# Optimization experiments

Measured on AMD Instinct MI355X. Metric: run time of the kernel, lower is better.

## Reference

```python
import jax, jax.numpy as jnp
import numpy as np

GROUP_SIZE = 64

def setup_inputs() -> dict:
    key = jax.random.key(0)
    ks = jax.random.split(key, 7)
    T, N, K, NG = 4096, 4096, 11264, 4096 // GROUP_SIZE
    x = jax.random.normal(ks[0], (T, N), dtype=jnp.float32)
    Q = jax.random.randint(ks[1], (K, N), 0, 8, dtype=jnp.int32)  # uint8 3-bit codes
    scales = jax.random.uniform(ks[2], (K, NG), dtype=jnp.float32)
    zeros = jax.random.uniform(ks[3], (K, NG), dtype=jnp.float32) * 7.0
    mu1 = jax.random.uniform(ks[4], (N,), dtype=jnp.float32) + 0.5
    mu2 = jax.random.uniform(ks[5], (K,), dtype=jnp.float32) + 0.5
    bias = jax.random.normal(ks[6], (K,), dtype=jnp.float32)
    return {"x": x, "Q": Q, "scales": scales, "zeros": zeros, "mu1": mu1, "mu2": mu2, "bias": bias}

def reference(x, Q, scales, zeros, mu1, mu2, bias):
    K, N = Q.shape
    ng = scales.shape[1]
    # group-wise dequant: (Q - zero) * scale, groups along N
    Qg = Q.astype(jnp.float32).reshape(K, ng, GROUP_SIZE)
    W_deq_norm = ((Qg - zeros[:, :, None]) * scales[:, :, None]).reshape(K, N)
    # Sinkhorn mu rescale: per-row mu2, per-column mu1
    W_deq = W_deq_norm * mu2[:, None] * mu1[None, :]
    out = x @ W_deq.T + bias
    return out
```

## Files before the change

kernel.cpp:

```cpp
#include <hip/hip_runtime.h>
#include <stdint.h>
#include <stddef.h>


typedef __attribute__((ext_vector_type(8))) short bfrag;
typedef __attribute__((ext_vector_type(4))) float f32x4;
typedef __attribute__((ext_vector_type(4))) int   i32x4;

__device__ __forceinline__ short f2bf(float f) {
    uint32_t u = __float_as_uint(f);
    u += 0x7fffu + ((u >> 16) & 1u);
    return (short)(u >> 16);
}

__device__ __forceinline__ void gload_lds16(const void* g, void* l) {
    __builtin_amdgcn_global_load_lds(
        (const __attribute__((address_space(1))) void*)g,
        (__attribute__((address_space(3))) void*)l,
        16, 0, 0);
}

__global__ void cvt_x_kernel(const float* __restrict__ x,
                             const float* __restrict__ mu1,
                             short* __restrict__ xb, int per ) {
    int i = blockIdx.x * 256 + threadIdx.x;
    int cb = (i % per) * 8;
    const f32x4* xv = (const f32x4*)x;
    f32x4 a = xv[2 * i];
    f32x4 b = xv[2 * i + 1];
    const f32x4* uv = (const f32x4*)(mu1 + cb);
    f32x4 u0 = uv[0];
    f32x4 u1 = uv[1];
    bfrag o;
    o[0] = f2bf(a[0] * u0[0]); o[1] = f2bf(a[1] * u0[1]);
    o[2] = f2bf(a[2] * u0[2]); o[3] = f2bf(a[3] * u0[3]);
    o[4] = f2bf(b[0] * u1[0]); o[5] = f2bf(b[1] * u1[1]);
    o[6] = f2bf(b[2] * u1[2]); o[7] = f2bf(b[3] * u1[3]);
    ((bfrag*)xb)[i] = o;
}

__global__ void deq_w_kernel(const int* __restrict__ Q,
                             const float* __restrict__ scales,
                             const float* __restrict__ zeros,
                             const float* __restrict__ mu2,
                             short* __restrict__ wb,
                             int k0, int N, int NG) {
    int kl = blockIdx.x;
    int kg = k0 + kl;
    int n0 = threadIdx.x << 4;
    int g  = n0 >> 6;
    float s = scales[(size_t)kg * NG + g] * mu2[kg];
    float z = zeros[(size_t)kg * NG + g];
    const i32x4* qv = (const i32x4*)(Q + (size_t)kg * N + n0);
    bfrag* wv = (bfrag*)(wb + (size_t)kl * N + n0);
#pragma unroll
    for (int h = 0; h < 2; h++) {
        i32x4 q0 = qv[2 * h];
        i32x4 q1 = qv[2 * h + 1];
        bfrag o;
        o[0] = f2bf(((float)q0[0] - z) * s);
        o[1] = f2bf(((float)q0[1] - z) * s);
        o[2] = f2bf(((float)q0[2] - z) * s);
        o[3] = f2bf(((float)q0[3] - z) * s);
        o[4] = f2bf(((float)q1[0] - z) * s);
        o[5] = f2bf(((float)q1[1] - z) * s);
        o[6] = f2bf(((float)q1[2] - z) * s);
        o[7] = f2bf(((float)q1[3] - z) * s);
        wv[h] = o;
    }
}

#define BM 128
#define BN 128
#define BK 32

__global__ void gemm_bt_kernel(const short* __restrict__ A,
                               const short* __restrict__ B,
                               const float* __restrict__ bias,
                               float* __restrict__ C,
                               int Kc, int Nout, int col0) {
    __shared__ __attribute__((aligned(16))) short As[BM * BK];
    __shared__ __attribute__((aligned(16))) short Bs[BN * BK];

    const int tid  = threadIdx.x;
    const int lane = tid & 63;
    const int wave = tid >> 6;
    const int wm   = (wave >> 1) * 64;
    const int wn   = (wave & 1) * 64;
    const int bm   = blockIdx.y * BM;
    const int bnl  = blockIdx.x * BN;

    f32x4 acc[4][4];
#pragma unroll
    for (int i = 0; i < 4; i++)
#pragma unroll
        for (int j = 0; j < 4; j++)
            acc[i][j] = (f32x4){0.f, 0.f, 0.f, 0.f};

    const int skc = ((tid & 3) ^ ((tid >> 3) & 3)) * 8;
    const short* gA  = A + (size_t)(bm + (tid >> 2)) * Kc + skc;
    const short* gA2 = gA + (size_t)64 * Kc;
    const short* gB  = B + (size_t)(bnl + (tid >> 2)) * Kc + skc;
    const short* gB2 = gB + (size_t)64 * Kc;
    short* lA  = As + tid * 8;
    short* lA2 = As + 2048 + tid * 8;
    short* lB  = Bs + tid * 8;
    short* lB2 = Bs + 2048 + tid * 8;

    const int r  = lane & 15;
    const int kc = lane >> 4;
    const int sw = (kc ^ ((r >> 1) & 3)) * 8;
    const short* pa = As + (wm + r) * BK + sw;
    const short* pb = Bs + (wn + r) * BK + sw;

    for (int k0 = 0; k0 < Kc; k0 += BK) {
        gload_lds16(gA + k0, lA);
        gload_lds16(gA2 + k0, lA2);
        gload_lds16(gB + k0, lB);
        gload_lds16(gB2 + k0, lB2);
        __syncthreads();

        bfrag af[4], bfv[4];
#pragma unroll
        for (int i = 0; i < 4; i++) af[i]  = *(const bfrag*)(pa + i * 16 * BK);
#pragma unroll
        for (int j = 0; j < 4; j++) bfv[j] = *(const bfrag*)(pb + j * 16 * BK);

#pragma unroll
        for (int i = 0; i < 4; i++)
#pragma unroll
            for (int j = 0; j < 4; j++)
                acc[i][j] = __builtin_amdgcn_mfma_f32_16x16x32_bf16(
                    af[i], bfv[j], acc[i][j], 0, 0, 0);

        __syncthreads();
    }

    const int row0  = bm + wm + (lane >> 4) * 4;
    const int colg0 = col0 + bnl + wn;
#pragma unroll
    for (int j = 0; j < 4; j++) {
        int col  = colg0 + j * 16 + r;
        float bv = bias[col];
#pragma unroll
        for (int i = 0; i < 4; i++) {
            int row = row0 + i * 16;
#pragma unroll
            for (int q = 0; q < 4; q++)
                C[(size_t)(row + q) * Nout + col] = acc[i][j][q] + bv;
        }
    }
}

__global__ void naive_kernel(const float* __restrict__ x, const int* __restrict__ Q,
                             const float* __restrict__ scales, const float* __restrict__ zeros,
                             const float* __restrict__ mu1, const float* __restrict__ mu2,
                             const float* __restrict__ bias, float* __restrict__ out,
                             int T, int N, int K, int NG) {
    long long total = (long long)T * K;
    for (long long idx = blockIdx.x * 256ll + threadIdx.x; idx < total;
         idx += (long long)gridDim.x * 256ll) {
        int t = (int)(idx / K);
        int k = (int)(idx - (long long)t * K);
        float s = 0.f;
        for (int n = 0; n < N; n++) {
            int g = n >> 6;
            float w = ((float)Q[(size_t)k * N + n] - zeros[(size_t)k * NG + g]) *
                      scales[(size_t)k * NG + g];
            s += x[(size_t)t * N + n] * w * mu1[n];
        }
        out[idx] = s * mu2[k] + bias[k];
    }
}

extern "C" void kernel_launch(void* const* d_in, const int* in_sizes, int n_in,
                              void* d_out, int out_size, void* d_ws, size_t ws_size,
                              hipStream_t stream) {
    const float* x      = (const float*)d_in[0];
    const int*   Q      = (const int*)d_in[1];
    const float* scales = (const float*)d_in[2];
    const float* zeros  = (const float*)d_in[3];
    const float* mu1    = (const float*)d_in[4];
    const float* mu2    = (const float*)d_in[5];
    const float* bias   = (const float*)d_in[6];
    float* out = (float*)d_out;

    const int N  = in_sizes[4];
    const int K  = in_sizes[5];
    const int T  = in_sizes[0] / N;
    const int NG = in_sizes[2] / K;

    const size_t xb_bytes  = (size_t)T * N * 2;
    const size_t row_bytes = (size_t)N * 2;

    if (ws_size < xb_bytes + 128 * row_bytes) {
        naive_kernel<<<4096, 256, 0, stream>>>(x, Q, scales, zeros, mu1, mu2,
                                               bias, out, T, N, K, NG);
        return;
    }

    short* xb = (short*)d_ws;
    short* wb = (short*)((char*)d_ws + xb_bytes);
    size_t max_rows = (ws_size - xb_bytes) / row_bytes;
    int CH = (int)((max_rows / 128) * 128);
    if (CH > K) CH = K;

    cvt_x_kernel<<<(T * N / 8) / 256, 256, 0, stream>>>(x, mu1, xb, N / 8);

    for (int c0 = 0; c0 < K; c0 += CH) {
        int rows = (K - c0 < CH) ? (K - c0) : CH;
        deq_w_kernel<<<rows, N / 16, 0, stream>>>(Q, scales, zeros, mu2, wb,
                                                  c0, N, NG);
        dim3 ggrid(rows / BN, T / BM);
        gemm_bt_kernel<<<ggrid, 256, 0, stream>>>(xb, wb, bias, out, N, K, c0);
    }
}
```

Baseline: 804.2 us.

## Fuse weight dequantization into GEMM B-tile loading with register prefetch

Removes the separate dequant kernel and its bf16 weight buffer. The GEMM now loads int32 codes plus per-group scale and zero directly and dequantizes into LDS inside the K loop. The next tile's codes are prefetched into registers to overlap global latency with compute, and a cheaper round-half-up bf16 conversion is used. In exchange, every M-block re-reads int32 codes, which are twice the size of bf16, and redoes the dequant ALU work. That adds global/L2 traffic and VALU pressure in the main loop.

```diff
diff --git a/kernel.cpp b/kernel.cpp
--- a/kernel.cpp
+++ b/kernel.cpp
@@ -11,6 +11,11 @@
     uint32_t u = __float_as_uint(f);
     u += 0x7fffu + ((u >> 16) & 1u);
     return (short)(u >> 16);
+}
+
+__device__ __forceinline__ short f2bfr(float f) {
+    uint32_t u = __float_as_uint(f);
+    return (short)((u + 0x8000u) >> 16);
 }
 
 __device__ __forceinline__ void gload_lds16(const void* g, void* l) {
@@ -39,46 +44,18 @@
     ((bfrag*)xb)[i] = o;
 }
 
-__global__ void deq_w_kernel(const int* __restrict__ Q,
-                             const float* __restrict__ scales,
-                             const float* __restrict__ zeros,
-                             const float* __restrict__ mu2,
-                             short* __restrict__ wb,
-                             int k0, int N, int NG) {
-    int kl = blockIdx.x;
-    int kg = k0 + kl;
-    int n0 = threadIdx.x << 4;
-    int g  = n0 >> 6;
-    float s = scales[(size_t)kg * NG + g] * mu2[kg];
-    float z = zeros[(size_t)kg * NG + g];
-    const i32x4* qv = (const i32x4*)(Q + (size_t)kg * N + n0);
-    bfrag* wv = (bfrag*)(wb + (size_t)kl * N + n0);
-#pragma unroll
-    for (int h = 0; h < 2; h++) {
-        i32x4 q0 = qv[2 * h];
-        i32x4 q1 = qv[2 * h + 1];
-        bfrag o;
-        o[0] = f2bf(((float)q0[0] - z) * s);
-        o[1] = f2bf(((float)q0[1] - z) * s);
-        o[2] = f2bf(((float)q0[2] - z) * s);
-        o[3] = f2bf(((float)q0[3] - z) * s);
-        o[4] = f2bf(((float)q1[0] - z) * s);
-        o[5] = f2bf(((float)q1[1] - z) * s);
-        o[6] = f2bf(((float)q1[2] - z) * s);
-        o[7] = f2bf(((float)q1[3] - z) * s);
-        wv[h] = o;
-    }
-}
-
 #define BM 128
 #define BN 128
 #define BK 32
 
-__global__ void gemm_bt_kernel(const short* __restrict__ A,
-                               const short* __restrict__ B,
-                               const float* __restrict__ bias,
-                               float* __restrict__ C,
-                               int Kc, int Nout, int col0) {
+__global__ void gemm_fused_kernel(const short* __restrict__ A,
+                                  const int* __restrict__ Q,
+                                  const float* __restrict__ scales,
+                                  const float* __restrict__ zeros,
+                                  const float* __restrict__ mu2,
+                                  const float* __restrict__ bias,
+                                  float* __restrict__ C,
+                                  int Kc, int Nout, int NG) {
     __shared__ __attribute__((aligned(16))) short As[BM * BK];
     __shared__ __attribute__((aligned(16))) short Bs[BN * BK];
 
@@ -88,7 +65,7 @@
     const int wm   = (wave >> 1) * 64;
     const int wn   = (wave & 1) * 64;
     const int bm   = blockIdx.y * BM;
-    const int bnl  = blockIdx.x * BN;
+    const int bn   = blockIdx.x * BN;
 
     f32x4 acc[4][4];
 #pragma unroll
@@ -100,12 +77,28 @@
     const int skc = ((tid & 3) ^ ((tid >> 3) & 3)) * 8;
     const short* gA  = A + (size_t)(bm + (tid >> 2)) * Kc + skc;
     const short* gA2 = gA + (size_t)64 * Kc;
-    const short* gB  = B + (size_t)(bnl + (tid >> 2)) * Kc + skc;
-    const short* gB2 = gB + (size_t)64 * Kc;
     short* lA  = As + tid * 8;
     short* lA2 = As + 2048 + tid * 8;
-    short* lB  = Bs + tid * 8;
-    short* lB2 = Bs + 2048 + tid * 8;
+
+    const int brow = tid >> 1;
+    const int bkh  = tid & 1;
+    const int krow = bn + brow;
+    const int* gq = Q + (size_t)krow * Kc + bkh * 16;
+    const float* sp = scales + (size_t)krow * NG;
+    const float* zp = zeros  + (size_t)krow * NG;
+    const float m2 = mu2[krow];
+    const int sw_b = (brow >> 1) & 3;
+    const int kc0  = 2 * bkh;
+    short* lB0 = Bs + ((size_t)brow * 4 + (kc0 ^ sw_b)) * 8;
+    short* lB1 = Bs + ((size_t)brow * 4 + ((kc0 + 1) ^ sw_b)) * 8;
+
+    i32x4 q0, q1, q2, q3;
+    {
+        const i32x4* qv = (const i32x4*)gq;
+        q0 = qv[0]; q1 = qv[1]; q2 = qv[2]; q3 = qv[3];
+    }
+    float s = sp[0] * m2;
+    float z = zp[0];
 
     const int r  = lane & 15;
     const int kc = lane >> 4;
@@ -116,8 +109,39 @@
     for (int k0 = 0; k0 < Kc; k0 += BK) {
         gload_lds16(gA + k0, lA);
         gload_lds16(gA2 + k0, lA2);
-        gload_lds16(gB + k0, lB);
-        gload_lds16(gB2 + k0, lB2);
+
+        i32x4 qn0 = q0, qn1 = q1, qn2 = q2, qn3 = q3;
+        float sn = s, zn = z;
+        int k1 = k0 + BK;
+        if (k1 < Kc) {
+            const i32x4* qv = (const i32x4*)(gq + k1);
+            qn0 = qv[0]; qn1 = qv[1]; qn2 = qv[2]; qn3 = qv[3];
+            if ((k1 & 63) == 0) {
+                sn = sp[k1 >> 6] * m2;
+                zn = zp[k1 >> 6];
+            }
+        }
+
+        bfrag o0, o1;
+        o0[0] = f2bfr(((float)q0[0] - z) * s);
+        o0[1] = f2bfr(((float)q0[1] - z) * s);
+        o0[2] = f2bfr(((float)q0[2] - z) * s);
+        o0[3] = f2bfr(((float)q0[3] - z) * s);
+        o0[4] = f2bfr(((float)q1[0] - z) * s);
+        o0[5] = f2bfr(((float)q1[1] - z) * s);
+        o0[6] = f2bfr(((float)q1[2] - z) * s);
+        o0[7] = f2bfr(((float)q1[3] - z) * s);
+        o1[0] = f2bfr(((float)q2[0] - z) * s);
+        o1[1] = f2bfr(((float)q2[1] - z) * s);
+        o1[2] = f2bfr(((float)q2[2] - z) * s);
+        o1[3] = f2bfr(((float)q2[3] - z) * s);
+        o1[4] = f2bfr(((float)q3[0] - z) * s);
+        o1[5] = f2bfr(((float)q3[1] - z) * s);
+        o1[6] = f2bfr(((float)q3[2] - z) * s);
+        o1[7] = f2bfr(((float)q3[3] - z) * s);
+        *(bfrag*)lB0 = o0;
+        *(bfrag*)lB1 = o1;
+
         __syncthreads();
 
         bfrag af[4], bfv[4];
@@ -134,10 +158,13 @@
                     af[i], bfv[j], acc[i][j], 0, 0, 0);
 
         __syncthreads();
+
+        q0 = qn0; q1 = qn1; q2 = qn2; q3 = qn3;
+        s = sn; z = zn;
     }
 
     const int row0  = bm + wm + (lane >> 4) * 4;
-    const int colg0 = col0 + bnl + wn;
+    const int colg0 = bn + wn;
 #pragma unroll
     for (int j = 0; j < 4; j++) {
         int col  = colg0 + j * 16 + r;
@@ -190,28 +217,18 @@
     const int T  = in_sizes[0] / N;
     const int NG = in_sizes[2] / K;
 
-    const size_t xb_bytes  = (size_t)T * N * 2;
-    const size_t row_bytes = (size_t)N * 2;
-
-    if (ws_size < xb_bytes + 128 * row_bytes) {
+    const size_t xb_bytes = (size_t)T * N * 2;
+
+    if (ws_size < xb_bytes) {
         naive_kernel<<<4096, 256, 0, stream>>>(x, Q, scales, zeros, mu1, mu2,
                                                bias, out, T, N, K, NG);
         return;
     }
 
     short* xb = (short*)d_ws;
-    short* wb = (short*)((char*)d_ws + xb_bytes);
-    size_t max_rows = (ws_size - xb_bytes) / row_bytes;
-    int CH = (int)((max_rows / 128) * 128);
-    if (CH > K) CH = K;
-
     cvt_x_kernel<<<(T * N / 8) / 256, 256, 0, stream>>>(x, mu1, xb, N / 8);
 
-    for (int c0 = 0; c0 < K; c0 += CH) {
-        int rows = (K - c0 < CH) ? (K - c0) : CH;
-        deq_w_kernel<<<rows, N / 16, 0, stream>>>(Q, scales, zeros, mu2, wb,
-                                                  c0, N, NG);
-        dim3 ggrid(rows / BN, T / BM);
-        gemm_bt_kernel<<<ggrid, 256, 0, stream>>>(xb, wb, bias, out, N, K, c0);
-    }
-}
+    dim3 ggrid(K / BN, T / BM);
+    gemm_fused_kernel<<<ggrid, 256, 0, stream>>>(xb, Q, scales, zeros, mu2,
+                                                 bias, out, N, K, NG);
+}
```

Result: slower. 1.161 ms (+44.4%).
